# Kernel tuning notes

Measured on AMD Instinct MI355X. Metric: run time of the kernel, lower is better.

## Reference

```python
import jax, jax.numpy as jnp
import numpy as np

B, H, S, D = 2, 16, 2048, 128


def alibi_slopes(n_heads: int) -> jnp.ndarray:
    # Standard ALiBi geometric slopes: 2^(-8*(h+1)/n_heads)
    h = jnp.arange(n_heads, dtype=jnp.float32)
    return jnp.exp2(-8.0 * (h + 1.0) / n_heads)


def setup_inputs() -> dict:
    key = jax.random.key(0)
    kq, kk, kv = jax.random.split(key, 3)
    q = jax.random.normal(kq, (B, H, S, D), dtype=jnp.float32)
    k = jax.random.normal(kk, (B, H, S, D), dtype=jnp.float32)
    v = jax.random.normal(kv, (B, H, S, D), dtype=jnp.float32)
    return {"q": q, "k": k, "v": v}


def reference(q, k, v):
    # FlexAttention forward: causal block mask + ALiBi score_mod, default scale 1/sqrt(D)
    d = q.shape[-1]
    scale = 1.0 / jnp.sqrt(jnp.asarray(d, dtype=q.dtype))
    slopes = alibi_slopes(q.shape[1]).astype(q.dtype)  # [H]

    scores = jnp.einsum("bhqd,bhkd->bhqk", q, k) * scale  # [B,H,S,S]
    q_idx = jnp.arange(q.shape[2])[:, None]   # [S,1]
    kv_idx = jnp.arange(k.shape[2])[None, :]  # [1,S]
    # score_mod: score + slopes[h] * (kv - q)  (bias <= 0 in causal region)
    bias = slopes[None, :, None, None] * (kv_idx - q_idx).astype(q.dtype)[None, None]
    scores = scores + bias
    causal = q_idx >= kv_idx  # [S,S]
    neg_inf = jnp.asarray(-jnp.inf, dtype=scores.dtype)
    scores = jnp.where(causal[None, None], scores, neg_inf)
    probs = jax.nn.softmax(scores, axis=-1)
    return jnp.einsum("bhqk,bhkd->bhqd", probs, v)
```

## Files before the change

kernel.cpp:

```cpp
#include <hip/hip_runtime.h>
#include <hip/hip_bf16.h>

#define BB 2
#define HH 16
#define SS 2048
#define DD 128

constexpr int BM = 64;
constexpr int BN = 64;
constexpr int NW = 4;
constexpr int PSTR = BN + 8;
constexpr size_t SD = (size_t)SS * DD;
constexpr size_t KV_ELEMS = (size_t)BB * HH * SS * DD;

typedef __bf16 bf16_t;
typedef __attribute__((ext_vector_type(8))) __bf16 bf16x8;
typedef __attribute__((ext_vector_type(4))) __bf16 bf16x4;
typedef __attribute__((ext_vector_type(4))) float floatx4;

__device__ __forceinline__ void dma16(const void* g, void* l) {
    __builtin_amdgcn_global_load_lds(
        (const __attribute__((address_space(1))) unsigned int*)g,
        (__attribute__((address_space(3))) unsigned int*)l,
        16, 0, 0);
}

__global__ __launch_bounds__(256)
void prep_kv(const float* __restrict__ kp, const float* __restrict__ vp,
             bf16_t* __restrict__ kbf, bf16_t* __restrict__ vtbf)
{
    __shared__ __align__(16) bf16_t VT[64][140];

    const int tid  = threadIdx.x;
    const int kv0  = blockIdx.x * BN;
    const size_t bh = blockIdx.y;

    const float* kb = kp + bh * SD;
    const float* vb = vp + bh * SD;
    bf16_t* ko = kbf  + bh * SD;
    bf16_t* vo = vtbf + bh * (size_t)DD * SS;

    #pragma unroll
    for (int i = 0; i < 8; ++i) {
        int idx4 = tid + i * 256;
        int row  = idx4 >> 5;
        int c4   = idx4 & 31;
        float4 val = *reinterpret_cast<const float4*>(vb + (size_t)(kv0 + row) * DD + c4 * 4);
        bf16x4 o;
        o[0] = (bf16_t)val.x; o[1] = (bf16_t)val.y; o[2] = (bf16_t)val.z; o[3] = (bf16_t)val.w;
        *reinterpret_cast<bf16x4*>(&VT[row][c4 * 4]) = o;
    }

    #pragma unroll
    for (int i = 0; i < 8; ++i) {
        int idx4 = tid + i * 256;
        int row  = idx4 >> 5;
        int c4   = idx4 & 31;
        float4 val = *reinterpret_cast<const float4*>(kb + (size_t)(kv0 + row) * DD + c4 * 4);
        bf16x4 o;
        o[0] = (bf16_t)val.x; o[1] = (bf16_t)val.y; o[2] = (bf16_t)val.z; o[3] = (bf16_t)val.w;
        *reinterpret_cast<bf16x4*>(ko + (size_t)(kv0 + row) * DD + c4 * 4) = o;
    }

    __syncthreads();

    const int kv8 = (tid & 7) * 8;
    const int dg  = tid >> 3;
    #pragma unroll
    for (int i = 0; i < 4; ++i) {
        int d = dg + i * 32;
        bf16x8 w;
        #pragma unroll
        for (int j = 0; j < 8; ++j)
            w[j] = VT[kv8 + j][d];
        *reinterpret_cast<bf16x8*>(vo + (size_t)d * SS + kv0 + kv8) = w;
    }
}

__global__ __launch_bounds__(256, 2)
void flexattn_fwd_bf16(const float* __restrict__ qp, const bf16_t* __restrict__ kbf,
                       const bf16_t* __restrict__ vtbf, float* __restrict__ op)
{
    __shared__ __align__(16) bf16_t KV[2][2][8192];
    __shared__ __align__(16) bf16_t QP[8192];
    bf16_t (*Ps)[16][PSTR] = reinterpret_cast<bf16_t(*)[16][PSTR]>(&QP[0]);

    const int tid  = threadIdx.x;
    const int wave = tid >> 6;
    const int lane = tid & 63;
    const int n16  = lane & 15;
    const int quad = lane >> 4;

    const int lid  = blockIdx.y * gridDim.x + blockIdx.x;
    const int xcd  = lid & 7;
    const int slot = lid >> 3;
    const int nl   = xcd * ((SS / BM) * BB * HH / 8) + slot;
    const int bh   = nl >> 5;
    const int qt   = 31 - (nl & 31);
    const int h    = bh & (HH - 1);
    const int q0   = qt * BM;

    const float LOG2E  = 1.4426950408889634f;
    const float sscale = 0.08838834764831845f * LOG2E;
    const float slope  = __builtin_amdgcn_exp2f(-8.0f * (float)(h + 1) / (float)HH);
    const float bscale = slope * LOG2E;

    const float*  qb = qp   + (size_t)bh * SD;
    const bf16_t* kb = kbf  + (size_t)bh * SD;
    const bf16_t* vt = vtbf + (size_t)bh * (size_t)DD * SS;
    float*        ob = op   + (size_t)bh * SD;

    int koff[4], voff[4];
    #pragma unroll
    for (int i = 0; i < 4; ++i) {
        int c   = wave * 256 + i * 64 + lane;
        int kv  = c >> 4;
        int col = (c & 15) ^ (kv & 15);
        koff[i] = kv * 256 + col * 16;
        int d  = c >> 3;
        int jp = c & 7;
        int j  = jp ^ (d & 7) ^ (((d >> 3) & 1) << 2);
        voff[i] = (d * SS + j * 8) * 2;
    }

    auto dma_tile = [&](int kt, int b) {
        const char* kg = (const char*)kb + (size_t)kt * (BN * DD * 2);
        const char* vg = (const char*)vt + (size_t)kt * (BN * 2);
        char* kl = (char*)&KV[b][0][0];
        char* vl = (char*)&KV[b][1][0];
        #pragma unroll
        for (int i = 0; i < 4; ++i) {
            int base = (wave * 256 + i * 64) * 16;
            dma16(kg + koff[i], kl + base);
            dma16(vg + voff[i], vl + base);
        }
    };

    #pragma unroll
    for (int i = 0; i < 8; ++i) {
        int idx4 = tid + i * 256;
        int row  = idx4 >> 5;
        int c4   = idx4 & 31;
        const float4 val = *reinterpret_cast<const float4*>(qb + (size_t)(q0 + row) * DD + c4 * 4);
        bf16x4 w;
        w[0] = (bf16_t)val.x; w[1] = (bf16_t)val.y; w[2] = (bf16_t)val.z; w[3] = (bf16_t)val.w;
        *reinterpret_cast<bf16x4*>(&QP[row * 128 + c4 * 4]) = w;
    }
    dma_tile(0, 0);
    __syncthreads();

    bf16x8 qf[4];
    #pragma unroll
    for (int c = 0; c < 4; ++c)
        qf[c] = *reinterpret_cast<const bf16x8*>(&QP[(wave * 16 + n16) * 128 + c * 32 + quad * 8]);
    __syncthreads();

    floatx4 o[8];
    #pragma unroll
    for (int t = 0; t < 8; ++t) o[t] = (floatx4){0.f, 0.f, 0.f, 0.f};
    float m_i = -3.0e38f, l_i = 0.f;

    const int bias_base = quad * 4 - (q0 + wave * 16 + n16);

    int kfo[4];
    #pragma unroll
    for (int c = 0; c < 4; ++c)
        kfo[c] = n16 * 256 + (((c * 4 + quad) ^ n16) * 16);
    const int vkey = (n16 & 7) ^ (((n16 >> 3) & 1) << 2);
    int vfo[2];
    #pragma unroll
    for (int c = 0; c < 2; ++c)
        vfo[c] = n16 * 128 + (((c * 4 + quad) ^ vkey) * 16);

    for (int kt = 0; kt <= qt; ++kt) {
        const int kv0 = kt * BN;
        const int b   = kt & 1;
        if (kt < qt) dma_tile(kt + 1, b ^ 1);

        const char* kl = (const char*)&KV[b][0][0];
        const char* vl = (const char*)&KV[b][1][0];

        floatx4 sc[4];
        __builtin_amdgcn_s_setprio(1);
        #pragma unroll
        for (int nt = 0; nt < 4; ++nt) {
            floatx4 acc = (floatx4){0.f, 0.f, 0.f, 0.f};
            #pragma unroll
            for (int c = 0; c < 4; ++c) {
                bf16x8 kf = *reinterpret_cast<const bf16x8*>(kl + nt * 4096 + kfo[c]);
                acc = __builtin_amdgcn_mfma_f32_16x16x32_bf16(kf, qf[c], acc, 0, 0, 0);
            }
            sc[nt] = acc;
        }
        __builtin_amdgcn_s_setprio(0);

        const bool diag = (kt == qt);
        float mloc = -3.0e38f;
        #pragma unroll
        for (int nt = 0; nt < 4; ++nt) {
            #pragma unroll
            for (int r = 0; r < 4; ++r) {
                int delta = kv0 + nt * 16 + r + bias_base;
                float sval = sc[nt][r] * sscale + bscale * (float)delta;
                if (diag && delta > 0) sval = -3.0e38f;
                sc[nt][r] = sval;
                mloc = fmaxf(mloc, sval);
            }
        }
        mloc = fmaxf(mloc, __shfl_xor(mloc, 16));
        mloc = fmaxf(mloc, __shfl_xor(mloc, 32));

        const bool grow = __any(mloc > m_i + 8.0f);
        float alpha = 1.0f;
        if (grow) {
            const float mnew = fmaxf(m_i, mloc);
            alpha = __builtin_amdgcn_exp2f(m_i - mnew);
            m_i = mnew;
        }

        float rs = 0.f;
        #pragma unroll
        for (int nt = 0; nt < 4; ++nt) {
            #pragma unroll
            for (int r = 0; r < 4; ++r) {
                float p = __builtin_amdgcn_exp2f(sc[nt][r] - m_i);
                sc[nt][r] = p;
                rs += p;
            }
        }
        rs += __shfl_xor(rs, 16);
        rs += __shfl_xor(rs, 32);
        l_i = l_i * alpha + rs;

        bf16x8 p0, p1;
        #pragma unroll
        for (int r = 0; r < 4; ++r) {
            p0[r]     = (bf16_t)sc[0][r];
            p0[r + 4] = (bf16_t)sc[1][r];
            p1[r]     = (bf16_t)sc[2][r];
            p1[r + 4] = (bf16_t)sc[3][r];
        }
        *reinterpret_cast<bf16x8*>(&Ps[wave][n16][quad * 16])     = p0;
        *reinterpret_cast<bf16x8*>(&Ps[wave][n16][quad * 16 + 8]) = p1;

        if (grow) {
            #pragma unroll
            for (int t = 0; t < 8; ++t) {
                #pragma unroll
                for (int r = 0; r < 4; ++r)
                    o[t][r] *= alpha;
            }
        }

        bf16x8 pf[2];
        #pragma unroll
        for (int c = 0; c < 2; ++c) {
            #pragma unroll
            for (int j4 = 0; j4 < 2; ++j4) {
                int s0 = (((2 * quad + j4) & 3) * 16) + ((2 * c + (quad >> 1)) * 4);
                bf16x4 ph = *reinterpret_cast<const bf16x4*>(&Ps[wave][n16][s0]);
                pf[c][j4 * 4 + 0] = ph[0];
                pf[c][j4 * 4 + 1] = ph[1];
                pf[c][j4 * 4 + 2] = ph[2];
                pf[c][j4 * 4 + 3] = ph[3];
            }
        }

        __builtin_amdgcn_s_setprio(1);
        #pragma unroll
        for (int t = 0; t < 8; ++t) {
            floatx4 acc = o[t];
            #pragma unroll
            for (int c = 0; c < 2; ++c) {
                bf16x8 vf = *reinterpret_cast<const bf16x8*>(vl + t * 2048 + vfo[c]);
                acc = __builtin_amdgcn_mfma_f32_16x16x32_bf16(vf, pf[c], acc, 0, 0, 0);
            }
            o[t] = acc;
        }
        __builtin_amdgcn_s_setprio(0);

        __syncthreads();
    }

    const float inv = 1.0f / l_i;
    const size_t rowoff = (size_t)(q0 + wave * 16 + n16) * DD;
    #pragma unroll
    for (int t = 0; t < 8; ++t) {
        float4 w;
        w.x = o[t][0] * inv; w.y = o[t][1] * inv;
        w.z = o[t][2] * inv; w.w = o[t][3] * inv;
        *reinterpret_cast<float4*>(ob + rowoff + t * 16 + quad * 4) = w;
    }
}

extern "C" void kernel_launch(void* const* d_in, const int* in_sizes, int n_in,
                              void* d_out, int out_size, void* d_ws, size_t ws_size,
                              hipStream_t stream) {
    const float* q = (const float*)d_in[0];
    const float* k = (const float*)d_in[1];
    const float* v = (const float*)d_in[2];
    float* out = (float*)d_out;

    bf16_t* kbf  = (bf16_t*)d_ws;
    bf16_t* vtbf = kbf + KV_ELEMS;
    prep_kv<<<dim3(SS / BN, BB * HH), 256, 0, stream>>>(k, v, kbf, vtbf);
    flexattn_fwd_bf16<<<dim3(SS / BM, BB * HH), 256, 0, stream>>>(q, kbf, vtbf, out);
}
```

Baseline: 219.4 us.

## Load K/V fragments directly from global memory instead of LDS double-buffering

```diff
diff --git a/kernel.cpp b/kernel.cpp
--- a/kernel.cpp
+++ b/kernel.cpp
@@ -17,13 +17,6 @@
 typedef __attribute__((ext_vector_type(8))) __bf16 bf16x8;
 typedef __attribute__((ext_vector_type(4))) __bf16 bf16x4;
 typedef __attribute__((ext_vector_type(4))) float floatx4;
-
-__device__ __forceinline__ void dma16(const void* g, void* l) {
-    __builtin_amdgcn_global_load_lds(
-        (const __attribute__((address_space(1))) unsigned int*)g,
-        (__attribute__((address_space(3))) unsigned int*)l,
-        16, 0, 0);
-}
 
 __global__ __launch_bounds__(256)
 void prep_kv(const float* __restrict__ kp, const float* __restrict__ vp,
@@ -77,13 +70,11 @@
     }
 }
 
-__global__ __launch_bounds__(256, 2)
+__global__ __launch_bounds__(256, 4)
 void flexattn_fwd_bf16(const float* __restrict__ qp, const bf16_t* __restrict__ kbf,
                        const bf16_t* __restrict__ vtbf, float* __restrict__ op)
 {
-    __shared__ __align__(16) bf16_t KV[2][2][8192];
-    __shared__ __align__(16) bf16_t QP[8192];
-    bf16_t (*Ps)[16][PSTR] = reinterpret_cast<bf16_t(*)[16][PSTR]>(&QP[0]);
+    __shared__ __align__(16) bf16_t Ps[NW][16][PSTR];
 
     const int tid  = threadIdx.x;
     const int wave = tid >> 6;
@@ -110,75 +101,30 @@
     const bf16_t* vt = vtbf + (size_t)bh * (size_t)DD * SS;
     float*        ob = op   + (size_t)bh * SD;
 
-    int koff[4], voff[4];
-    #pragma unroll
-    for (int i = 0; i < 4; ++i) {
-        int c   = wave * 256 + i * 64 + lane;
-        int kv  = c >> 4;
-        int col = (c & 15) ^ (kv & 15);
-        koff[i] = kv * 256 + col * 16;
-        int d  = c >> 3;
-        int jp = c & 7;
-        int j  = jp ^ (d & 7) ^ (((d >> 3) & 1) << 2);
-        voff[i] = (d * SS + j * 8) * 2;
-    }
-
-    auto dma_tile = [&](int kt, int b) {
-        const char* kg = (const char*)kb + (size_t)kt * (BN * DD * 2);
-        const char* vg = (const char*)vt + (size_t)kt * (BN * 2);
-        char* kl = (char*)&KV[b][0][0];
-        char* vl = (char*)&KV[b][1][0];
-        #pragma unroll
-        for (int i = 0; i < 4; ++i) {
-            int base = (wave * 256 + i * 64) * 16;
-            dma16(kg + koff[i], kl + base);
-            dma16(vg + voff[i], vl + base);
-        }
-    };
-
-    #pragma unroll
-    for (int i = 0; i < 8; ++i) {
-        int idx4 = tid + i * 256;
-        int row  = idx4 >> 5;
-        int c4   = idx4 & 31;
-        const float4 val = *reinterpret_cast<const float4*>(qb + (size_t)(q0 + row) * DD + c4 * 4);
-        bf16x4 w;
-        w[0] = (bf16_t)val.x; w[1] = (bf16_t)val.y; w[2] = (bf16_t)val.z; w[3] = (bf16_t)val.w;
-        *reinterpret_cast<bf16x4*>(&QP[row * 128 + c4 * 4]) = w;
-    }
-    dma_tile(0, 0);
-    __syncthreads();
+    const int q = q0 + wave * 16 + n16;
 
     bf16x8 qf[4];
     #pragma unroll
-    for (int c = 0; c < 4; ++c)
-        qf[c] = *reinterpret_cast<const bf16x8*>(&QP[(wave * 16 + n16) * 128 + c * 32 + quad * 8]);
-    __syncthreads();
+    for (int c = 0; c < 4; ++c) {
+        const float* qs = qb + (size_t)q * DD + c * 32 + quad * 8;
+        float4 a = *reinterpret_cast<const float4*>(qs);
+        float4 b = *reinterpret_cast<const float4*>(qs + 4);
+        qf[c][0] = (bf16_t)a.x; qf[c][1] = (bf16_t)a.y;
+        qf[c][2] = (bf16_t)a.z; qf[c][3] = (bf16_t)a.w;
+        qf[c][4] = (bf16_t)b.x; qf[c][5] = (bf16_t)b.y;
+        qf[c][6] = (bf16_t)b.z; qf[c][7] = (bf16_t)b.w;
+    }
 
     floatx4 o[8];
     #pragma unroll
     for (int t = 0; t < 8; ++t) o[t] = (floatx4){0.f, 0.f, 0.f, 0.f};
     float m_i = -3.0e38f, l_i = 0.f;
 
-    const int bias_base = quad * 4 - (q0 + wave * 16 + n16);
-
-    int kfo[4];
-    #pragma unroll
-    for (int c = 0; c < 4; ++c)
-        kfo[c] = n16 * 256 + (((c * 4 + quad) ^ n16) * 16);
-    const int vkey = (n16 & 7) ^ (((n16 >> 3) & 1) << 2);
-    int vfo[2];
-    #pragma unroll
-    for (int c = 0; c < 2; ++c)
-        vfo[c] = n16 * 128 + (((c * 4 + quad) ^ vkey) * 16);
+    const int bias_base = quad * 4 - q;
 
     for (int kt = 0; kt <= qt; ++kt) {
         const int kv0 = kt * BN;
-        const int b   = kt & 1;
-        if (kt < qt) dma_tile(kt + 1, b ^ 1);
-
-        const char* kl = (const char*)&KV[b][0][0];
-        const char* vl = (const char*)&KV[b][1][0];
+        const bf16_t* ktile = kb + (size_t)kv0 * DD;
 
         floatx4 sc[4];
         __builtin_amdgcn_s_setprio(1);
@@ -187,7 +133,8 @@
             floatx4 acc = (floatx4){0.f, 0.f, 0.f, 0.f};
             #pragma unroll
             for (int c = 0; c < 4; ++c) {
-                bf16x8 kf = *reinterpret_cast<const bf16x8*>(kl + nt * 4096 + kfo[c]);
+                bf16x8 kf = *reinterpret_cast<const bf16x8*>(
+                    ktile + (size_t)(nt * 16 + n16) * DD + c * 32 + quad * 8);
                 acc = __builtin_amdgcn_mfma_f32_16x16x32_bf16(kf, qf[c], acc, 0, 0, 0);
             }
             sc[nt] = acc;
@@ -272,18 +219,17 @@
             floatx4 acc = o[t];
             #pragma unroll
             for (int c = 0; c < 2; ++c) {
-                bf16x8 vf = *reinterpret_cast<const bf16x8*>(vl + t * 2048 + vfo[c]);
+                bf16x8 vf = *reinterpret_cast<const bf16x8*>(
+                    vt + (size_t)(t * 16 + n16) * SS + kv0 + c * 32 + quad * 8);
                 acc = __builtin_amdgcn_mfma_f32_16x16x32_bf16(vf, pf[c], acc, 0, 0, 0);
             }
             o[t] = acc;
         }
         __builtin_amdgcn_s_setprio(0);
-
-        __syncthreads();
     }
 
     const float inv = 1.0f / l_i;
-    const size_t rowoff = (size_t)(q0 + wave * 16 + n16) * DD;
+    const size_t rowoff = (size_t)q * DD;
     #pragma unroll
     for (int t = 0; t < 8; ++t) {
         float4 w;
```

Result: slower. 577.2 us (+163.0%).
